# Optimization experiments

Measured on AMD Instinct MI355X. Metric: run time of the kernel, lower is better.

The kernel has to match this reference:

```python
import jax, jax.numpy as jnp
import numpy as np

HEADS = 24
HEAD_DIM = 128
DIM = HEADS * HEAD_DIM  # 3072
EPS = 1e-5


def _rms_norm(x, w):
    # x: [B,S,H,D], w: [D]
    var = jnp.mean(jnp.square(x), axis=-1, keepdims=True)
    return x * jax.lax.rsqrt(var + EPS) * w


def _apply_rope(x, cos, sin):
    # non-neox (interleaved pairs): x: [B,S,H,D], cos/sin: [S,D]
    B, S, H, D = x.shape
    xr = x.reshape(B, S, H, D // 2, 2)
    x_real, x_imag = xr[..., 0], xr[..., 1]
    rotated = jnp.stack([-x_imag, x_real], axis=-1).reshape(B, S, H, D)
    c = cos[None, :, None, :]
    s = sin[None, :, None, :]
    return x * c + rotated * s


def setup_inputs() -> dict:
    key = jax.random.key(0)
    ks = jax.random.split(key, 20)
    B, S_img, S_txt = 1, 2048, 512
    S = S_img + S_txt
    sc = 1.0 / np.sqrt(DIM)
    inp = {
        "x": jax.random.normal(ks[0], (B, S_img, DIM), jnp.float32),
        "encoder_hidden_states": jax.random.normal(ks[1], (B, S_txt, DIM), jnp.float32),
        "rope_cos": jax.random.uniform(ks[2], (S, HEAD_DIM), jnp.float32),
        "rope_sin": jax.random.uniform(ks[3], (S, HEAD_DIM), jnp.float32),
        # image-stream projections (bias=False)
        "wq": jax.random.normal(ks[4], (DIM, DIM), jnp.float32) * sc,
        "wk": jax.random.normal(ks[5], (DIM, DIM), jnp.float32) * sc,
        "wv": jax.random.normal(ks[6], (DIM, DIM), jnp.float32) * sc,
        # text-stream projections (added_proj_bias=True)
        "w_add_q": jax.random.normal(ks[7], (DIM, DIM), jnp.float32) * sc,
        "w_add_k": jax.random.normal(ks[8], (DIM, DIM), jnp.float32) * sc,
        "w_add_v": jax.random.normal(ks[9], (DIM, DIM), jnp.float32) * sc,
        "b_add_q": jax.random.normal(ks[10], (DIM,), jnp.float32) * 0.01,
        "b_add_k": jax.random.normal(ks[11], (DIM,), jnp.float32) * 0.01,
        "b_add_v": jax.random.normal(ks[12], (DIM,), jnp.float32) * 0.01,
        # per-head RMSNorm weights
        "norm_q_w": jnp.ones((HEAD_DIM,), jnp.float32),
        "norm_k_w": jnp.ones((HEAD_DIM,), jnp.float32),
        "norm_aq_w": jnp.ones((HEAD_DIM,), jnp.float32),
        "norm_ak_w": jnp.ones((HEAD_DIM,), jnp.float32),
        # output projections (out_bias=True)
        "w_out": jax.random.normal(ks[13], (DIM, DIM), jnp.float32) * sc,
        "b_out": jax.random.normal(ks[14], (DIM,), jnp.float32) * 0.01,
        "w_add_out": jax.random.normal(ks[15], (DIM, DIM), jnp.float32) * sc,
        "b_add_out": jax.random.normal(ks[16], (DIM,), jnp.float32) * 0.01,
    }
    return inp


def reference(x, encoder_hidden_states, rope_cos, rope_sin,
              wq, wk, wv, w_add_q, w_add_k, w_add_v,
              b_add_q, b_add_k, b_add_v,
              norm_q_w, norm_k_w, norm_aq_w, norm_ak_w,
              w_out, b_out, w_add_out, b_add_out):
    B, S_img, _ = x.shape
    S_txt = encoder_hidden_states.shape[1]

    def proj(h, w, b=None):
        y = jnp.einsum('bsd,ed->bse', h, w)
        return y if b is None else y + b

    def heads(t):
        return t.reshape(B, t.shape[1], HEADS, HEAD_DIM)

    q = _rms_norm(heads(proj(x, wq)), norm_q_w)
    k = _rms_norm(heads(proj(x, wk)), norm_k_w)
    v = heads(proj(x, wv))

    eq = _rms_norm(heads(proj(encoder_hidden_states, w_add_q, b_add_q)), norm_aq_w)
    ek = _rms_norm(heads(proj(encoder_hidden_states, w_add_k, b_add_k)), norm_ak_w)
    ev = heads(proj(encoder_hidden_states, w_add_v, b_add_v))

    # encoder tokens first, then image tokens
    q = jnp.concatenate([eq, q], axis=1)
    k = jnp.concatenate([ek, k], axis=1)
    v = jnp.concatenate([ev, v], axis=1)

    q = _apply_rope(q, rope_cos, rope_sin)
    k = _apply_rope(k, rope_cos, rope_sin)

    scale = 1.0 / np.sqrt(HEAD_DIM)
    scores = jnp.einsum('bqhd,bkhd->bhqk', q, k) * scale
    attn = jax.nn.softmax(scores, axis=-1)
    o = jnp.einsum('bhqk,bkhd->bqhd', attn, v)
    o = o.reshape(B, S_txt + S_img, DIM)

    enc_o, img_o = o[:, :S_txt], o[:, S_txt:]
    img_out = jnp.einsum('bsd,ed->bse', img_o, w_out) + b_out
    enc_out = jnp.einsum('bsd,ed->bse', enc_o, w_add_out) + b_add_out
    return img_out, enc_out
```

## Files before the change

kernel.cpp:

```cpp
#include <hip/hip_runtime.h>
#include <hip/hip_bf16.h>


typedef __hip_bfloat16 bf16;
typedef __attribute__((ext_vector_type(8))) short short8;
typedef __attribute__((ext_vector_type(4))) short s16x4;
typedef __attribute__((ext_vector_type(4))) float f32x4;

#define KDIM 3072
#define S_TXT 512
#define S_IMG 2048
#define S_ALL 2560
#define NHEADS 24
#define HDIM 128
#define WELEM (KDIM * KDIM)
#define AELEM (S_ALL * KDIM)
#define NSPLIT 3
#define NT_K 48
#define QBN 192

__device__ __forceinline__ void async_ld16(const void* g, void* l) {
  __builtin_amdgcn_global_load_lds((__attribute__((address_space(1))) void*)g,
                                   (__attribute__((address_space(3))) void*)l,
                                   16, 0, 0);
}

__device__ __forceinline__ short bf16_bits(float x) {
  bf16 h = (bf16)x;
  return __builtin_bit_cast(short, h);
}
__device__ __forceinline__ float bits_f32(short s) {
  return (float)__builtin_bit_cast(bf16, s);
}

__device__ __forceinline__ void phase_mid() {
  __builtin_amdgcn_s_barrier();
  asm volatile("s_waitcnt lgkmcnt(0)" ::: "memory");
  __builtin_amdgcn_sched_barrier(0);
  __builtin_amdgcn_s_setprio(1);
}
__device__ __forceinline__ void phase_end() {
  __builtin_amdgcn_s_setprio(0);
  __builtin_amdgcn_s_barrier();
}

__global__ __launch_bounds__(256) void cast_weights_kernel(
    const float* __restrict__ w0, const float* __restrict__ w1,
    const float* __restrict__ w2, const float* __restrict__ w3,
    const float* __restrict__ w4, const float* __restrict__ w5,
    const float* __restrict__ w6, const float* __restrict__ w7,
    bf16* __restrict__ dst) {
  const float* srcs[8] = {w0, w1, w2, w3, w4, w5, w6, w7};
  const float* __restrict__ src = srcs[blockIdx.y];
  bf16* __restrict__ out = dst + (size_t)blockIdx.y * WELEM;
  const size_t i0 = ((size_t)blockIdx.x * 256 + threadIdx.x) * 8;
  const float4 f0 = *(const float4*)(src + i0);
  const float4 f1 = *(const float4*)(src + i0 + 4);
  short8 o;
  o[0] = bf16_bits(f0.x); o[1] = bf16_bits(f0.y);
  o[2] = bf16_bits(f0.z); o[3] = bf16_bits(f0.w);
  o[4] = bf16_bits(f1.x); o[5] = bf16_bits(f1.y);
  o[6] = bf16_bits(f1.z); o[7] = bf16_bits(f1.w);
  *(short8*)(out + i0) = o;
}

__global__ __launch_bounds__(256) void cast_acts_kernel(
    const float* __restrict__ x, const float* __restrict__ enc,
    bf16* __restrict__ xe) {
  const size_t i0 = ((size_t)blockIdx.x * 256 + threadIdx.x) * 8;
  const size_t TXT = (size_t)S_TXT * KDIM;
  const float* __restrict__ src = (i0 < TXT) ? (enc + i0) : (x + (i0 - TXT));
  const float4 f0 = *(const float4*)(src);
  const float4 f1 = *(const float4*)(src + 4);
  short8 o;
  o[0] = bf16_bits(f0.x); o[1] = bf16_bits(f0.y);
  o[2] = bf16_bits(f0.z); o[3] = bf16_bits(f0.w);
  o[4] = bf16_bits(f1.x); o[5] = bf16_bits(f1.y);
  o[6] = bf16_bits(f1.z); o[7] = bf16_bits(f1.w);
  *(short8*)(xe + i0) = o;
}

template <typename OutT, bool TRANS>
__device__ __forceinline__ void gemm256(const bf16* __restrict__ Ab,
                                        const bf16* __restrict__ Bb,
                                        OutT* __restrict__ C,
                                        const float* __restrict__ bias,
                                        short* sAmem, short* sBmem) {
  const int tid = threadIdx.x;
  const int lane = tid & 63;
  const int w = tid >> 6;
  const int a = lane & 15;
  const int g = (lane >> 4) & 3;
  const int wm = w >> 1;
  const int wn = w & 1;

  short* const A00 = sAmem;
  short* const A01 = sAmem + 8192;
  short* const A10 = sAmem + 16384;
  short* const A11 = sAmem + 24576;
  short* const B00 = sBmem;
  short* const B01 = sBmem + 6144;
  short* const B10 = sBmem + 12288;
  short* const B11 = sBmem + 18432;

  auto stageA = [&](int kbase, short* lblk) {
#pragma unroll
    for (int l = 0; l < 2; l++) {
      const int t = l * 512 + tid;
      const int row = t >> 2;
      const int ls = (t & 3) ^ ((row >> 1) & 3);
      async_ld16(Ab + (size_t)row * KDIM + kbase + ls * 8,
                 lblk + (l * 512 + w * 64) * 8);
    }
  };
  auto stageB = [&](int kbase, short* lblk) {
    {
      const int t = tid;
      const int row = t >> 2;
      const int ls = (t & 3) ^ ((row >> 1) & 3);
      async_ld16(Bb + (size_t)row * KDIM + kbase + ls * 8,
                 lblk + (w * 64) * 8);
    }
    if (w < 4) {
      const int t = 512 + tid;
      const int row = t >> 2;
      const int ls = (t & 3) ^ ((row >> 1) & 3);
      async_ld16(Bb + (size_t)row * KDIM + kbase + ls * 8,
                 lblk + (512 + w * 64) * 8);
    }
  };
  auto frag = [&](const short* lblk, int R) -> short8 {
    return *(const short8*)(lblk + R * 32 + ((g ^ ((R >> 1) & 3)) * 8));
  };

  f32x4 acc[4][6] = {};

  stageB(0, B00);
  stageA(0, A00);
  stageB(32, B01);
  stageA(32, A01);
  stageA(64, A10);
  stageB(64, B10);
  asm volatile("s_waitcnt vmcnt(3)" ::: "memory");
  __builtin_amdgcn_s_barrier();

  const int ra = wm * 64 + a;
  const int rb = wn * 96 + a;

  auto kblock = [&](int u, short* cA0, short* cA1, short* cB0, short* cB1,
                    short* nA1, short* nB1) {
    short8 af[4], bfr[3];
#pragma unroll
    for (int i = 0; i < 4; i++) af[i] = frag(cA0, ra + i * 16);
#pragma unroll
    for (int j = 0; j < 3; j++) bfr[j] = frag(cB0, rb + j * 16);
    if (u + 1 < NT_K) {
      stageA((u + 1) * 64 + 32, nA1);
      stageB((u + 1) * 64 + 32, nB1);
    }
    phase_mid();
#pragma unroll
    for (int i = 0; i < 4; i++)
#pragma unroll
      for (int j = 0; j < 3; j++)
        acc[i][j] = __builtin_amdgcn_mfma_f32_16x16x32_bf16(af[i], bfr[j], acc[i][j], 0, 0, 0);
    phase_end();
#pragma unroll
    for (int j = 0; j < 3; j++) bfr[j] = frag(cB0, rb + (j + 3) * 16);
    if (u + 2 < NT_K) stageA((u + 2) * 64, cA0);
    phase_mid();
#pragma unroll
    for (int i = 0; i < 4; i++)
#pragma unroll
      for (int j = 0; j < 3; j++)
        acc[i][j + 3] = __builtin_amdgcn_mfma_f32_16x16x32_bf16(af[i], bfr[j], acc[i][j + 3], 0, 0, 0);
    phase_end();
#pragma unroll
    for (int i = 0; i < 4; i++) af[i] = frag(cA1, ra + i * 16);
#pragma unroll
    for (int j = 0; j < 3; j++) bfr[j] = frag(cB1, rb + j * 16);
    if (u + 2 < NT_K) stageB((u + 2) * 64, cB0);
    phase_mid();
#pragma unroll
    for (int i = 0; i < 4; i++)
#pragma unroll
      for (int j = 0; j < 3; j++)
        acc[i][j] = __builtin_amdgcn_mfma_f32_16x16x32_bf16(af[i], bfr[j], acc[i][j], 0, 0, 0);
    phase_end();
#pragma unroll
    for (int j = 0; j < 3; j++) bfr[j] = frag(cB1, rb + (j + 3) * 16);
    __builtin_amdgcn_s_barrier();
    asm volatile("s_waitcnt lgkmcnt(0)" ::: "memory");
    __builtin_amdgcn_sched_barrier(0);
    __builtin_amdgcn_s_setprio(1);
#pragma unroll
    for (int i = 0; i < 4; i++)
#pragma unroll
      for (int j = 0; j < 3; j++)
        acc[i][j + 3] = __builtin_amdgcn_mfma_f32_16x16x32_bf16(af[i], bfr[j], acc[i][j + 3], 0, 0, 0);
    __builtin_amdgcn_s_setprio(0);
    if (u < NT_K - 2)
      asm volatile("s_waitcnt vmcnt(3)" ::: "memory");
    else
      asm volatile("s_waitcnt vmcnt(0)" ::: "memory");
    __builtin_amdgcn_s_barrier();
  };

#pragma unroll 1
  for (int u = 0; u < NT_K; u += 2) {
    kblock(u,     A00, A01, B00, B01, A11, B11);
    kblock(u + 1, A10, A11, B10, B11, A01, B01);
  }

  if constexpr (TRANS) {
#pragma unroll
    for (int i = 0; i < 4; i++)
#pragma unroll
      for (int j = 0; j < 6; j++) {
        const int col = wn * 96 + j * 16 + a;
        const float bv = bias ? bias[col] : 0.0f;
        s16x4 pk;
#pragma unroll
        for (int r = 0; r < 4; r++) pk[r] = bf16_bits(acc[i][j][r] + bv);
        *(s16x4*)((short*)C + (size_t)col * S_ALL + wm * 64 + i * 16 + g * 4) = pk;
      }
  } else {
#pragma unroll
    for (int i = 0; i < 4; i++)
#pragma unroll
      for (int j = 0; j < 6; j++) {
        const int col = wn * 96 + j * 16 + a;
        const float bv = bias ? bias[col] : 0.0f;
#pragma unroll
        for (int r = 0; r < 4; r++) {
          const int row = wm * 64 + i * 16 + g * 4 + r;
          C[(size_t)row * KDIM + col] = (OutT)(acc[i][j][r] + bv);
        }
      }
  }
}

__global__ __launch_bounds__(512, 2) void qkv_kernel(
    const bf16* __restrict__ XE, const bf16* __restrict__ Wc,
    const float* __restrict__ bq, const float* __restrict__ bk, const float* __restrict__ bv,
    bf16* __restrict__ Q, bf16* __restrict__ K, bf16* __restrict__ VT) {
  __shared__ alignas(16) short sAmem[4 * 8192];
  __shared__ alignas(16) short sBmem[4 * 6144];
  const int bid = blockIdx.x;
  const int wk_ = (bid & 7) * 60 + (bid >> 3);
  const int bm = wk_ / 48;
  const int bn = wk_ % 48;
  const int which = bn / 16;
  const int nc = (bn % 16) * QBN;
  const bool txt = bm < 2;
  const bf16* W = Wc + (size_t)(txt ? (3 + which) : which) * WELEM + (size_t)nc * KDIM;
  const float* bias = nullptr;
  if (txt) bias = ((which == 0) ? bq : (which == 1) ? bk : bv) + nc;
  const int crow = bm * 256;
  const bf16* A = XE + (size_t)crow * KDIM;
  if (which == 2) {
    gemm256<bf16, true>(A, W, VT + (size_t)nc * S_ALL + crow, bias, sAmem, sBmem);
  } else {
    bf16* Out = (which == 0) ? Q : K;
    gemm256<bf16, false>(A, W, Out + (size_t)crow * KDIM + nc, bias, sAmem, sBmem);
  }
}

template <typename OutT, bool TRANS>
__device__ __forceinline__ void gemm_tile(const bf16* __restrict__ A,
                                          const bf16* __restrict__ B,
                                          OutT* __restrict__ C,
                                          const float* __restrict__ bias) {
  __shared__ alignas(16) short sA[128 * 32];
  __shared__ alignas(16) short sB[128 * 32];
  const int tid = threadIdx.x;
  const int lane = tid & 63;
  const int w = tid >> 6;
  const int a = lane & 15;
  const int g = lane >> 4;
  const int wm = (w >> 1) * 64;
  const int wn = (w & 1) * 64;

  f32x4 acc[4][4] = {};

  const int s0 = tid, s1 = tid + 256;
  const int r0 = s0 >> 2, b0 = (s0 & 3) ^ ((r0 >> 1) & 3);
  const int r1 = s1 >> 2, b1 = (s1 & 3) ^ ((r1 >> 1) & 3);
  const bf16* gA0 = A + (size_t)r0 * KDIM + b0 * 8;
  const bf16* gA1 = A + (size_t)r1 * KDIM + b1 * 8;
  const bf16* gB0 = B + (size_t)r0 * KDIM + b0 * 8;
  const bf16* gB1 = B + (size_t)r1 * KDIM + b1 * 8;
  short* lA0 = sA + (w * 64) * 8;
  short* lA1 = sA + (256 + w * 64) * 8;
  short* lB0 = sB + (w * 64) * 8;
  short* lB1 = sB + (256 + w * 64) * 8;

  for (int k0 = 0; k0 < KDIM; k0 += 32) {
    __syncthreads();
    async_ld16(gA0 + k0, lA0);
    async_ld16(gA1 + k0, lA1);
    async_ld16(gB0 + k0, lB0);
    async_ld16(gB1 + k0, lB1);
    __syncthreads();
    short8 af[4], bfg[4];
#pragma unroll
    for (int i = 0; i < 4; i++) {
      const int R = wm + i * 16 + a;
      af[i] = *(const short8*)(sA + R * 32 + ((g ^ ((R >> 1) & 3)) * 8));
    }
#pragma unroll
    for (int j = 0; j < 4; j++) {
      const int R = wn + j * 16 + a;
      bfg[j] = *(const short8*)(sB + R * 32 + ((g ^ ((R >> 1) & 3)) * 8));
    }
#pragma unroll
    for (int i = 0; i < 4; i++)
#pragma unroll
      for (int j = 0; j < 4; j++)
        acc[i][j] = __builtin_amdgcn_mfma_f32_16x16x32_bf16(af[i], bfg[j], acc[i][j], 0, 0, 0);
  }

  if constexpr (TRANS) {
#pragma unroll
    for (int i = 0; i < 4; i++)
#pragma unroll
      for (int j = 0; j < 4; j++) {
        const int col = wn + j * 16 + a;
        const float bv = bias ? bias[col] : 0.0f;
        s16x4 pk;
#pragma unroll
        for (int r = 0; r < 4; r++) pk[r] = bf16_bits(acc[i][j][r] + bv);
        *(s16x4*)((short*)C + (size_t)col * S_ALL + wm + i * 16 + g * 4) = pk;
      }
  } else {
#pragma unroll
    for (int i = 0; i < 4; i++)
#pragma unroll
      for (int j = 0; j < 4; j++) {
        const int col = wn + j * 16 + a;
        const float bv = bias ? bias[col] : 0.0f;
#pragma unroll
        for (int r = 0; r < 4; r++) {
          const int row = wm + i * 16 + g * 4 + r;
          C[(size_t)row * KDIM + col] = (OutT)(acc[i][j][r] + bv);
        }
      }
  }
}

__global__ __launch_bounds__(256) void outproj_kernel(
    const bf16* __restrict__ Obuf, const bf16* __restrict__ Wc,
    const float* __restrict__ b_out, const float* __restrict__ b_add,
    float* __restrict__ out) {
  const int bm = blockIdx.x;
  const int bn = blockIdx.y;
  const bool txt = bm < 4;
  const bf16* A = Obuf + (size_t)bm * 128 * KDIM;
  const bf16* W = Wc + (size_t)(txt ? 7 : 6) * WELEM;
  const float* bias = txt ? b_add : b_out;
  float* C = txt ? (out + (size_t)S_IMG * KDIM + (size_t)bm * 128 * KDIM)
                 : (out + (size_t)(bm - 4) * 128 * KDIM);
  gemm_tile<float, false>(A, W + (size_t)bn * 128 * KDIM, C + bn * 128, bias + bn * 128);
}

__global__ __launch_bounds__(256) void norm_rope_kernel(
    bf16* __restrict__ Q, bf16* __restrict__ K,
    const float* __restrict__ rc, const float* __restrict__ rs,
    const float* __restrict__ nqw, const float* __restrict__ nkw,
    const float* __restrict__ naqw, const float* __restrict__ nakw) {
  const int row = blockIdx.x;
  const int h = blockIdx.y * 4 + (threadIdx.x >> 6);
  const int t = threadIdx.x & 63;
  const long base = (long)row * KDIM + h * HDIM;
  const int d0 = 2 * t, d1 = d0 + 1;
  const bool txt = row < S_TXT;
  const float QSCL = 0.08838834764831845f * 1.4426950408889634f;
  float qa = (float)Q[base + d0], qb = (float)Q[base + d1];
  float ka = (float)K[base + d0], kb = (float)K[base + d1];
  float sq = qa * qa + qb * qb;
  float sk = ka * ka + kb * kb;
#pragma unroll
  for (int m = 1; m < 64; m <<= 1) {
    sq += __shfl_xor(sq, m);
    sk += __shfl_xor(sk, m);
  }
  const float rq = rsqrtf(sq * (1.0f / 128.0f) + 1e-5f) * QSCL;
  const float rk = rsqrtf(sk * (1.0f / 128.0f) + 1e-5f);
  const float* qw = txt ? naqw : nqw;
  const float* kw = txt ? nakw : nkw;
  const float c0 = rc[row * HDIM + d0], c1 = rc[row * HDIM + d1];
  const float s0 = rs[row * HDIM + d0], s1 = rs[row * HDIM + d1];
  const float qn0 = qa * rq * qw[d0], qn1 = qb * rq * qw[d1];
  const float kn0 = ka * rk * kw[d0], kn1 = kb * rk * kw[d1];
  Q[base + d0] = (bf16)(qn0 * c0 - qn1 * s0);
  Q[base + d1] = (bf16)(qn1 * c1 + qn0 * s1);
  K[base + d0] = (bf16)(kn0 * c0 - kn1 * s0);
  K[base + d1] = (bf16)(kn1 * c1 + kn0 * s1);
}

__global__ __launch_bounds__(256) void flash_kernel(
    const bf16* __restrict__ Q, const bf16* __restrict__ Kb,
    const bf16* __restrict__ VT,
    bf16* __restrict__ Op0, bf16* __restrict__ Op1, bf16* __restrict__ Op2,
    float* __restrict__ L) {
  __shared__ alignas(16) short sK[64 * 128];
  __shared__ alignas(16) short sVT[128 * 64];
  __shared__ alignas(16) short sP[4][32 * 72];
  const int tid = threadIdx.x;
  const int lane = tid & 63;
  const int w = tid >> 6;
  const int a = lane & 15;
  const int g = lane >> 4;
  const int qt = blockIdx.x;
  const int h = blockIdx.y;
  const int split = blockIdx.z;
  const int it0 = split * 13;
  const int it1 = (split == 2) ? 40 : (it0 + 13);
  const int qrow0 = qt * 128 + w * 32;
  short* const sPw = sP[w];

  short8 qf[2][4];
#pragma unroll
  for (int mi = 0; mi < 2; mi++)
#pragma unroll
    for (int kk = 0; kk < 4; kk++)
      qf[mi][kk] = *(const short8*)(Q + (size_t)(qrow0 + mi * 16 + a) * KDIM + h * HDIM + kk * 32 + g * 8);

  f32x4 oacc[2][8] = {};
  float lsum[2] = {0.0f, 0.0f};

  for (int it = it0; it < it1; ++it) {
    const int kv0 = it * 64;
    __syncthreads();
#pragma unroll
    for (int is = 0; is < 4; is++) {
      const int s = is * 256 + w * 64 + lane;
      const int kr = s >> 4, p = s & 15;
      const int lb = (p - (kr & 7)) & 15;
      async_ld16(Kb + (size_t)(kv0 + kr) * KDIM + h * HDIM + lb * 8,
                 sK + (is * 256 + w * 64) * 8);
    }
#pragma unroll
    for (int is = 0; is < 4; is++) {
      const int s = is * 256 + w * 64 + lane;
      const int dr = s >> 3, p = s & 7;
      const int lb = (p - (dr & 7)) & 7;
      async_ld16(VT + (size_t)(h * HDIM + dr) * S_ALL + kv0 + lb * 8,
                 sVT + (is * 256 + w * 64) * 8);
    }
    __syncthreads();

    f32x4 st[4][2] = {};
#pragma unroll
    for (int kk = 0; kk < 4; kk++) {
      short8 kf[4];
#pragma unroll
      for (int ni = 0; ni < 4; ni++) {
        const int kr = ni * 16 + a;
        const int p = ((kk * 4 + g) + (kr & 7)) & 15;
        kf[ni] = *(const short8*)(sK + kr * 128 + p * 8);
      }
#pragma unroll
      for (int ni = 0; ni < 4; ni++)
#pragma unroll
        for (int mi = 0; mi < 2; mi++)
          st[ni][mi] = __builtin_amdgcn_mfma_f32_16x16x32_bf16(kf[ni], qf[mi][kk], st[ni][mi], 0, 0, 0);
    }

#pragma unroll
    for (int mi = 0; mi < 2; mi++)
#pragma unroll
      for (int ni = 0; ni < 4; ni++) {
        s16x4 pk;
#pragma unroll
        for (int r = 0; r < 4; r++) {
          const float p = exp2f(st[ni][mi][r]);
          lsum[mi] += p;
          pk[r] = bf16_bits(p);
        }
        *(s16x4*)(sPw + (mi * 16 + a) * 72 + ni * 16 + g * 4) = pk;
      }

#pragma unroll
    for (int ks = 0; ks < 2; ks++) {
      short8 pf[2];
#pragma unroll
      for (int mi = 0; mi < 2; mi++)
        pf[mi] = *(const short8*)(sPw + (mi * 16 + a) * 72 + ks * 32 + g * 8);
#pragma unroll
      for (int nd = 0; nd < 8; nd++) {
        const int dr = nd * 16 + a;
        const int p = ((ks * 4 + g) + (dr & 7)) & 7;
        const short8 vf = *(const short8*)(sVT + dr * 64 + p * 8);
#pragma unroll
        for (int mi = 0; mi < 2; mi++)
          oacc[mi][nd] = __builtin_amdgcn_mfma_f32_16x16x32_bf16(pf[mi], vf, oacc[mi][nd], 0, 0, 0);
      }
    }
  }

#pragma unroll
  for (int mi = 0; mi < 2; mi++) {
    lsum[mi] += __shfl_xor(lsum[mi], 16);
    lsum[mi] += __shfl_xor(lsum[mi], 32);
  }
  bf16* __restrict__ Op = (split == 0) ? Op0 : (split == 1) ? Op1 : Op2;
#pragma unroll
  for (int mi = 0; mi < 2; mi++) {
#pragma unroll
    for (int r = 0; r < 4; r++) {
      const float inv = 1.0f / __shfl(lsum[mi], g * 4 + r);
      const size_t row = qrow0 + mi * 16 + g * 4 + r;
#pragma unroll
      for (int nd = 0; nd < 8; nd++)
        Op[row * KDIM + h * HDIM + nd * 16 + a] = (bf16)(oacc[mi][nd][r] * inv);
    }
    if (g == 0)
      L[((size_t)split * NHEADS + h) * S_ALL + qrow0 + mi * 16 + a] = lsum[mi];
  }
}

__global__ __launch_bounds__(256) void merge_kernel(
    bf16* __restrict__ O0, const bf16* __restrict__ O1, const bf16* __restrict__ O2,
    const float* __restrict__ L) {
  const size_t i0 = ((size_t)blockIdx.x * 256 + threadIdx.x) * 8;
  const int row = (int)(i0 / KDIM);
  const int h = (int)((i0 % KDIM) >> 7);
  const float l0 = L[((size_t)0 * NHEADS + h) * S_ALL + row];
  const float l1 = L[((size_t)1 * NHEADS + h) * S_ALL + row];
  const float l2 = L[((size_t)2 * NHEADS + h) * S_ALL + row];
  const float inv = 1.0f / (l0 + l1 + l2);
  const float w0 = l0 * inv, w1 = l1 * inv, w2 = l2 * inv;
  const short8 v0 = *(const short8*)(O0 + i0);
  const short8 v1 = *(const short8*)(O1 + i0);
  const short8 v2 = *(const short8*)(O2 + i0);
  short8 o;
#pragma unroll
  for (int u = 0; u < 8; u++)
    o[u] = bf16_bits(w0 * bits_f32(v0[u]) + w1 * bits_f32(v1[u]) + w2 * bits_f32(v2[u]));
  *(short8*)(O0 + i0) = o;
}

extern "C" void kernel_launch(void* const* d_in, const int* in_sizes, int n_in,
                              void* d_out, int out_size, void* d_ws, size_t ws_size,
                              hipStream_t stream) {
  const float* x    = (const float*)d_in[0];
  const float* enc  = (const float*)d_in[1];
  const float* rc   = (const float*)d_in[2];
  const float* rs   = (const float*)d_in[3];
  const float* wq   = (const float*)d_in[4];
  const float* wk   = (const float*)d_in[5];
  const float* wv   = (const float*)d_in[6];
  const float* waq  = (const float*)d_in[7];
  const float* wak  = (const float*)d_in[8];
  const float* wav  = (const float*)d_in[9];
  const float* bq   = (const float*)d_in[10];
  const float* bk   = (const float*)d_in[11];
  const float* bv   = (const float*)d_in[12];
  const float* nqw  = (const float*)d_in[13];
  const float* nkw  = (const float*)d_in[14];
  const float* naqw = (const float*)d_in[15];
  const float* nakw = (const float*)d_in[16];
  const float* w_out     = (const float*)d_in[17];
  const float* b_out     = (const float*)d_in[18];
  const float* w_add_out = (const float*)d_in[19];
  const float* b_add_out = (const float*)d_in[20];

  bf16* Wc   = (bf16*)d_ws;
  bf16* XE   = Wc + (size_t)8 * WELEM;
  bf16* Q    = XE + AELEM;
  bf16* K    = Q + AELEM;
  bf16* VT   = K + AELEM;
  bf16* Obuf = VT + AELEM;
  bf16* Op1  = Obuf + AELEM;
  bf16* Op2  = XE;
  float* L   = (float*)(Op1 + AELEM);

  cast_weights_kernel<<<dim3(WELEM / 2048, 8), 256, 0, stream>>>(
      wq, wk, wv, waq, wak, wav, w_out, w_add_out, Wc);
  cast_acts_kernel<<<dim3(AELEM / 2048), 256, 0, stream>>>(x, enc, XE);

  qkv_kernel<<<dim3(480), dim3(512), 0, stream>>>(XE, Wc, bq, bk, bv, Q, K, VT);
  norm_rope_kernel<<<dim3(S_ALL, 6), 256, 0, stream>>>(Q, K, rc, rs, nqw, nkw, naqw, nakw);
  flash_kernel<<<dim3(20, NHEADS, NSPLIT), 256, 0, stream>>>(Q, K, VT, Obuf, Op1, Op2, L);
  merge_kernel<<<dim3(AELEM / 2048), 256, 0, stream>>>(Obuf, Op1, Op2, L);
  outproj_kernel<<<dim3(20, NHEADS), 256, 0, stream>>>(Obuf, Wc, b_out, b_add_out,
                                                       (float*)d_out);
}
```

Baseline: 738.5 us.

## Restructure GEMM main loop into double-buffered k-tiles with one barrier per tile

Replaces the four-phase ping-pong loop, which had a barrier between every MFMA group, with a plain double-buffered scheme. Each k-tile of 64 now reads all of its LDS fragments up front, issues async global-to-LDS loads for the next full tile into the other buffer, and uses graduated lgkmcnt waits so MFMA groups start as their fragments arrive. There is one vmcnt(0) and barrier per tile. This cuts barrier and synchronisation overhead, but holds more fragment registers live and waits for all global loads at the end of every tile, so prefetch depth is lower.

```diff
diff --git a/kernel.cpp b/kernel.cpp
--- a/kernel.cpp
+++ b/kernel.cpp
@@ -31,17 +31,6 @@
 }
 __device__ __forceinline__ float bits_f32(short s) {
   return (float)__builtin_bit_cast(bf16, s);
-}
-
-__device__ __forceinline__ void phase_mid() {
-  __builtin_amdgcn_s_barrier();
-  asm volatile("s_waitcnt lgkmcnt(0)" ::: "memory");
-  __builtin_amdgcn_sched_barrier(0);
-  __builtin_amdgcn_s_setprio(1);
-}
-__device__ __forceinline__ void phase_end() {
-  __builtin_amdgcn_s_setprio(0);
-  __builtin_amdgcn_s_barrier();
 }
 
 __global__ __launch_bounds__(256) void cast_weights_kernel(
@@ -94,14 +83,14 @@
   const int wm = w >> 1;
   const int wn = w & 1;
 
-  short* const A00 = sAmem;
-  short* const A01 = sAmem + 8192;
-  short* const A10 = sAmem + 16384;
-  short* const A11 = sAmem + 24576;
-  short* const B00 = sBmem;
-  short* const B01 = sBmem + 6144;
-  short* const B10 = sBmem + 12288;
-  short* const B11 = sBmem + 18432;
+  short* const A0h0 = sAmem;
+  short* const A0h1 = sAmem + 8192;
+  short* const A1h0 = sAmem + 16384;
+  short* const A1h1 = sAmem + 24576;
+  short* const B0h0 = sBmem;
+  short* const B0h1 = sBmem + 6144;
+  short* const B1h0 = sBmem + 12288;
+  short* const B1h1 = sBmem + 18432;
 
   auto stageA = [&](int kbase, short* lblk) {
 #pragma unroll
@@ -135,61 +124,74 @@
 
   f32x4 acc[4][6] = {};
 
-  stageB(0, B00);
-  stageA(0, A00);
-  stageB(32, B01);
-  stageA(32, A01);
-  stageA(64, A10);
-  stageB(64, B10);
-  asm volatile("s_waitcnt vmcnt(3)" ::: "memory");
+  stageA(0, A0h0);
+  stageA(32, A0h1);
+  stageB(0, B0h0);
+  stageB(32, B0h1);
+  asm volatile("s_waitcnt vmcnt(0)" ::: "memory");
   __builtin_amdgcn_s_barrier();
 
   const int ra = wm * 64 + a;
   const int rb = wn * 96 + a;
 
-  auto kblock = [&](int u, short* cA0, short* cA1, short* cB0, short* cB1,
-                    short* nA1, short* nB1) {
-    short8 af[4], bfr[3];
-#pragma unroll
-    for (int i = 0; i < 4; i++) af[i] = frag(cA0, ra + i * 16);
-#pragma unroll
-    for (int j = 0; j < 3; j++) bfr[j] = frag(cB0, rb + j * 16);
+  auto ktile = [&](int u, const short* cA0, const short* cA1,
+                   const short* cB0, const short* cB1,
+                   short* nA0, short* nA1, short* nB0, short* nB1) {
+    short8 af0[4], af1[4], b0a[3], b0b[3], b1a[3], b1b[3];
+#pragma unroll
+    for (int i = 0; i < 4; i++) af0[i] = frag(cA0, ra + i * 16);
+#pragma unroll
+    for (int j = 0; j < 3; j++) b0a[j] = frag(cB0, rb + j * 16);
+    __builtin_amdgcn_sched_barrier(0);
+#pragma unroll
+    for (int j = 0; j < 3; j++) b0b[j] = frag(cB0, rb + (j + 3) * 16);
+    __builtin_amdgcn_sched_barrier(0);
+#pragma unroll
+    for (int i = 0; i < 4; i++) af1[i] = frag(cA1, ra + i * 16);
+#pragma unroll
+    for (int j = 0; j < 3; j++) b1a[j] = frag(cB1, rb + j * 16);
+    __builtin_amdgcn_sched_barrier(0);
+#pragma unroll
+    for (int j = 0; j < 3; j++) b1b[j] = frag(cB1, rb + (j + 3) * 16);
+    __builtin_amdgcn_sched_barrier(0);
     if (u + 1 < NT_K) {
-      stageA((u + 1) * 64 + 32, nA1);
-      stageB((u + 1) * 64 + 32, nB1);
-    }
-    phase_mid();
+      const int kb = (u + 1) * 64;
+      stageA(kb, nA0);
+      stageA(kb + 32, nA1);
+      stageB(kb, nB0);
+      stageB(kb + 32, nB1);
+    }
+    __builtin_amdgcn_sched_barrier(0);
+    asm volatile("s_waitcnt lgkmcnt(13)" ::: "memory");
+    __builtin_amdgcn_sched_barrier(0);
+    __builtin_amdgcn_s_setprio(1);
 #pragma unroll
     for (int i = 0; i < 4; i++)
 #pragma unroll
       for (int j = 0; j < 3; j++)
-        acc[i][j] = __builtin_amdgcn_mfma_f32_16x16x32_bf16(af[i], bfr[j], acc[i][j], 0, 0, 0);
-    phase_end();
-#pragma unroll
-    for (int j = 0; j < 3; j++) bfr[j] = frag(cB0, rb + (j + 3) * 16);
-    if (u + 2 < NT_K) stageA((u + 2) * 64, cA0);
-    phase_mid();
+        acc[i][j] = __builtin_amdgcn_mfma_f32_16x16x32_bf16(af0[i], b0a[j], acc[i][j], 0, 0, 0);
+    __builtin_amdgcn_s_setprio(0);
+    __builtin_amdgcn_sched_barrier(0);
+    asm volatile("s_waitcnt lgkmcnt(10)" ::: "memory");
+    __builtin_amdgcn_sched_barrier(0);
+    __builtin_amdgcn_s_setprio(1);
 #pragma unroll
     for (int i = 0; i < 4; i++)
 #pragma unroll
       for (int j = 0; j < 3; j++)
-        acc[i][j + 3] = __builtin_amdgcn_mfma_f32_16x16x32_bf16(af[i], bfr[j], acc[i][j + 3], 0, 0, 0);
-    phase_end();
-#pragma unroll
-    for (int i = 0; i < 4; i++) af[i] = frag(cA1, ra + i * 16);
-#pragma unroll
-    for (int j = 0; j < 3; j++) bfr[j] = frag(cB1, rb + j * 16);
-    if (u + 2 < NT_K) stageB((u + 2) * 64, cB0);
-    phase_mid();
+        acc[i][j + 3] = __builtin_amdgcn_mfma_f32_16x16x32_bf16(af0[i], b0b[j], acc[i][j + 3], 0, 0, 0);
+    __builtin_amdgcn_s_setprio(0);
+    __builtin_amdgcn_sched_barrier(0);
+    asm volatile("s_waitcnt lgkmcnt(3)" ::: "memory");
+    __builtin_amdgcn_sched_barrier(0);
+    __builtin_amdgcn_s_setprio(1);
 #pragma unroll
     for (int i = 0; i < 4; i++)
 #pragma unroll
       for (int j = 0; j < 3; j++)
-        acc[i][j] = __builtin_amdgcn_mfma_f32_16x16x32_bf16(af[i], bfr[j], acc[i][j], 0, 0, 0);
-    phase_end();
-#pragma unroll
-    for (int j = 0; j < 3; j++) bfr[j] = frag(cB1, rb + (j + 3) * 16);
-    __builtin_amdgcn_s_barrier();
+        acc[i][j] = __builtin_amdgcn_mfma_f32_16x16x32_bf16(af1[i], b1a[j], acc[i][j], 0, 0, 0);
+    __builtin_amdgcn_s_setprio(0);
+    __builtin_amdgcn_sched_barrier(0);
     asm volatile("s_waitcnt lgkmcnt(0)" ::: "memory");
     __builtin_amdgcn_sched_barrier(0);
     __builtin_amdgcn_s_setprio(1);
@@ -197,19 +199,17 @@
     for (int i = 0; i < 4; i++)
 #pragma unroll
       for (int j = 0; j < 3; j++)
-        acc[i][j + 3] = __builtin_amdgcn_mfma_f32_16x16x32_bf16(af[i], bfr[j], acc[i][j + 3], 0, 0, 0);
+        acc[i][j + 3] = __builtin_amdgcn_mfma_f32_16x16x32_bf16(af1[i], b1b[j], acc[i][j + 3], 0, 0, 0);
     __builtin_amdgcn_s_setprio(0);
-    if (u < NT_K - 2)
-      asm volatile("s_waitcnt vmcnt(3)" ::: "memory");
-    else
-      asm volatile("s_waitcnt vmcnt(0)" ::: "memory");
+    __builtin_amdgcn_sched_barrier(0);
+    asm volatile("s_waitcnt vmcnt(0)" ::: "memory");
     __builtin_amdgcn_s_barrier();
   };
 
 #pragma unroll 1
   for (int u = 0; u < NT_K; u += 2) {
-    kblock(u,     A00, A01, B00, B01, A11, B11);
-    kblock(u + 1, A10, A11, B10, B11, A01, B01);
+    ktile(u,     A0h0, A0h1, B0h0, B0h1, A1h0, A1h1, B1h0, B1h1);
+    ktile(u + 1, A1h0, A1h1, B1h0, B1h1, A0h0, A0h1, B0h0, B0h1);
   }
 
   if constexpr (TRANS) {
```

After: 736.8 us. About the same (-0.2%).
